# Performance work log

Measured on AMD Instinct MI355X. Metric: run time of the kernel, lower is better.

## Reference

```python
import jax, jax.numpy as jnp
import numpy as np

VOCAB_SIZES = [100000] * 26
EMBED_DIM = 128
BOT_DIMS = [512, 256, 128]
TOP_DIMS = [1024, 1024, 512, 256, 1]
N_DENSE = 13
BATCH = 8192


def setup_inputs() -> dict:
    key = jax.random.key(0)
    ks = jax.random.split(key, 32)
    inp = {}
    inp['dense_features'] = jax.random.normal(ks[0], (BATCH, N_DENSE), dtype=jnp.float32)
    inp['cat_features'] = jax.random.randint(ks[1], (BATCH, 26), 0, VOCAB_SIZES[0], dtype=jnp.int32)
    total_vocab = sum(VOCAB_SIZES)
    inp['embedding_table'] = jax.random.uniform(ks[2], (total_vocab, EMBED_DIM), dtype=jnp.float32,
                                               minval=-1.0, maxval=1.0) * (3.0 / EMBED_DIM) ** 0.5
    # Bottom MLP params
    fan_in = N_DENSE
    for i, d in enumerate(BOT_DIMS):
        inp[f'W{i}'] = jax.random.normal(ks[3 + i], (fan_in, d), dtype=jnp.float32) * (2.0 / (fan_in + d)) ** 0.5
        inp[f'b{i}'] = jax.random.normal(ks[8 + i], (d,), dtype=jnp.float32) * (1.0 / d) ** 0.5
        fan_in = d
    # Top MLP params; input dim = 128 + 27*28/2 = 506
    n_feat = 1 + len(VOCAB_SIZES)
    fan_in = BOT_DIMS[-1] + n_feat * (n_feat + 1) // 2
    for i, d in enumerate(TOP_DIMS):
        inp[f'T{i}'] = jax.random.normal(ks[14 + i], (fan_in, d), dtype=jnp.float32) * (2.0 / (fan_in + d)) ** 0.5
        inp[f'tb{i}'] = jax.random.normal(ks[22 + i], (d,), dtype=jnp.float32) * (1.0 / d) ** 0.5
        fan_in = d
    return inp


def reference(dense_features, cat_features, embedding_table,
              W0, b0, W1, b1, W2, b2,
              T0, tb0, T1, tb1, T2, tb2, T3, tb3, T4, tb4):
    B = dense_features.shape[0]
    # Bottom MLP
    x = dense_features
    for W, b in ((W0, b0), (W1, b1), (W2, b2)):
        x = jax.nn.relu(x @ W + b)
    bot_out = x  # [B, 128]
    feature_stack = bot_out.reshape(B, -1, EMBED_DIM)  # [B, 1, 128]
    # Embedding lookup with per-table offsets into concatenated table
    offsets = jnp.asarray(np.concatenate([[0], np.cumsum(VOCAB_SIZES[:-1])]), dtype=jnp.int32)
    idx = (cat_features + offsets[None, :]).reshape(-1)
    embed = embedding_table[idx].reshape(B, len(VOCAB_SIZES), EMBED_DIM)  # [B, 26, 128]
    feats = jnp.concatenate([feature_stack, embed], axis=1)  # [B, 27, 128]
    # Dot interaction: upper-triangular (incl. diag) entries of feats @ feats^T
    xactions = jnp.einsum('bnd,bmd->bnm', feats, feats)  # [B, 27, 27]
    iu, ju = jnp.triu_indices(feats.shape[1])
    dot_out = xactions[:, iu, ju]  # [B, 378] row-major upper-tri, same order as boolean-mask extraction
    top_in = jnp.concatenate([bot_out, dot_out], axis=-1)  # [B, 506]
    # Top MLP: relu on all but last layer, sigmoid on last
    tops = ((T0, tb0), (T1, tb1), (T2, tb2), (T3, tb3), (T4, tb4))
    x = top_in
    for i, (W, b) in enumerate(tops):
        x = x @ W + b
        x = jax.nn.sigmoid(x) if i == len(tops) - 1 else jax.nn.relu(x)
    return x
```

## Files before the change

kernel.cpp:

```cpp
#include <hip/hip_runtime.h>
#include <hip/hip_bf16.h>
#include <math.h>

#define BATCH 8192

typedef __bf16 bf16x8 __attribute__((ext_vector_type(8)));
typedef float f32x4 __attribute__((ext_vector_type(4)));

__device__ __forceinline__ unsigned short f2bf(float f) {
    unsigned int u = __float_as_uint(f);
    u = u + 0x7FFFu + ((u >> 16) & 1u);
    return (unsigned short)(u >> 16);
}
__device__ __forceinline__ float bf2f(unsigned short h) {
    return __uint_as_float(((unsigned int)h) << 16);
}
__device__ __forceinline__ void async16(const void* g, void* l) {
    __builtin_amdgcn_global_load_lds(
        (const __attribute__((address_space(1))) unsigned int*)g,
        (__attribute__((address_space(3))) unsigned int*)l, 16, 0, 0);
}

__global__ __launch_bounds__(256) void bottom13_kernel(
    const float* __restrict__ dense,
    const float* __restrict__ W0, const float* __restrict__ b0,
    unsigned short* __restrict__ h1)
{
    __shared__ float xs[8][16];
    const int t = threadIdx.x;
    const int row0 = blockIdx.x * 8;

    if (t < 8 * 13) {
        int r = t / 13, k = t % 13;
        xs[r][k] = dense[(size_t)(row0 + r) * 13 + k];
    }
    __syncthreads();

    #pragma unroll
    for (int jj = 0; jj < 2; ++jj) {
        const int j = t + jj * 256;
        float acc[8];
        const float bj = b0[j];
        #pragma unroll
        for (int r = 0; r < 8; ++r) acc[r] = bj;
        #pragma unroll
        for (int k = 0; k < 13; ++k) {
            float w = W0[k * 512 + j];
            #pragma unroll
            for (int r = 0; r < 8; ++r) acc[r] += xs[r][k] * w;
        }
        #pragma unroll
        for (int r = 0; r < 8; ++r)
            h1[(size_t)(row0 + r) * 512 + j] = f2bf(fmaxf(acc[r], 0.f));
    }
}

struct TransDesc { const float* W; unsigned short* Wt; int K, N, nkb, tile0; };
struct TransDescs { TransDesc d[6]; };

__global__ __launch_bounds__(256) void trans_all_kernel(TransDescs td)
{
    __shared__ float tile[32][33];
    const int b = blockIdx.x;
    int i = 0;
    #pragma unroll
    for (int q = 1; q < 6; ++q) if (b >= td.d[q].tile0) i = q;
    const TransDesc D = td.d[i];
    const int tl = b - D.tile0;
    const int kb = (tl % D.nkb) * 32;
    const int nb = (tl / D.nkb) * 32;
    const int Kpad = D.nkb * 32;
    const int tx = threadIdx.x & 31, ty = threadIdx.x >> 5;

    #pragma unroll
    for (int r = 0; r < 32; r += 8) {
        int k = kb + ty + r;
        tile[ty + r][tx] = (k < D.K) ? D.W[(size_t)k * D.N + nb + tx] : 0.f;
    }
    __syncthreads();
    #pragma unroll
    for (int r = 0; r < 32; r += 8) {
        D.Wt[(size_t)(nb + ty + r) * Kpad + kb + tx] = f2bf(tile[tx][ty + r]);
    }
}

__global__ __launch_bounds__(256) void interact_kernel(
    const int* __restrict__ cat,
    const float* __restrict__ table,
    const float* __restrict__ botf,
    unsigned short* __restrict__ A0)
{
    __shared__ float fs[27][132];
    __shared__ int idx[26];

    const int t = threadIdx.x;
    const int row = blockIdx.x;

    if (t < 26) idx[t] = cat[(size_t)row * 26 + t] + t * 100000;
    __syncthreads();

    for (int q = t; q < 27 * 32; q += 256) {
        const int i  = q >> 5;
        const int c4 = q & 31;
        const float* src = (i == 0) ? (botf + (size_t)row * 128)
                                    : (table + (size_t)idx[i - 1] * 128);
        float4 v = reinterpret_cast<const float4*>(src)[c4];
        fs[i][c4 * 4 + 0] = v.x;
        fs[i][c4 * 4 + 1] = v.y;
        fs[i][c4 * 4 + 2] = v.z;
        fs[i][c4 * 4 + 3] = v.w;
    }
    __syncthreads();

    for (int p = t; p < 378; p += 256) {
        int i = 0, rem = p;
        while (rem >= 27 - i) { rem -= 27 - i; ++i; }
        const int j = i + rem;
        float s = 0.f;
        for (int k = 0; k < 128; k += 4) {
            float4 a = *reinterpret_cast<const float4*>(&fs[i][k]);
            float4 b = *reinterpret_cast<const float4*>(&fs[j][k]);
            s += a.x * b.x + a.y * b.y + a.z * b.z + a.w * b.w;
        }
        A0[(size_t)row * 512 + 128 + p] = f2bf(s);
    }
    if (t < 6) A0[(size_t)row * 512 + 506 + t] = 0;
}

__global__ __launch_bounds__(256) void gemm_bf16_kernel(
    const unsigned short* __restrict__ A,
    const unsigned short* __restrict__ Bt,
    const float* __restrict__ bias,
    unsigned short* __restrict__ C,
    float* __restrict__ Cf,
    int K, int N, int ldc, int relu)
{
    __shared__ unsigned short As[2][128 * 64];
    __shared__ unsigned short Bs[2][128 * 64];

    const int t = threadIdx.x;
    const int lane = t & 63;
    const int wid = t >> 6;
    const int wr = wid >> 1, wc = wid & 1;
    const int row0 = blockIdx.x * 128;
    const int col0 = blockIdx.y * 128;

    const char* gA[4]; const char* gB[4];
    int ldst[4];
    #pragma unroll
    for (int q = 0; q < 4; ++q) {
        int l16 = q * 256 + t;
        int row = l16 >> 3, chunk = l16 & 7;
        int swz = chunk ^ (row & 7);
        gA[q] = (const char*)A  + ((size_t)(row0 + row) * K + swz * 8) * 2;
        gB[q] = (const char*)Bt + ((size_t)(col0 + row) * K + swz * 8) * 2;
        ldst[q] = l16 * 16;
    }

    const int kb = lane >> 4;
    const int r15 = lane & 15;
    int aoff[4][2], boff[4][2];
    #pragma unroll
    for (int m = 0; m < 4; ++m) {
        int r = wr * 64 + m * 16 + r15;
        int c = wc * 64 + m * 16 + r15;
        #pragma unroll
        for (int ks = 0; ks < 2; ++ks) {
            aoff[m][ks] = r * 128 + (((ks * 4 + kb) ^ (r & 7)) << 4);
            boff[m][ks] = c * 128 + (((ks * 4 + kb) ^ (c & 7)) << 4);
        }
    }

    f32x4 acc[4][4] = {};

    const int nt = K >> 6;

    #pragma unroll
    for (int q = 0; q < 4; ++q) {
        async16(gA[q], (char*)As[0] + ldst[q]);
        async16(gB[q], (char*)Bs[0] + ldst[q]);
    }
    __syncthreads();

    int cur = 0;
    for (int tt = 0; tt < nt; ++tt) {
        if (tt + 1 < nt) {
            const size_t koff = (size_t)(tt + 1) * 64 * 2;
            #pragma unroll
            for (int q = 0; q < 4; ++q) {
                async16(gA[q] + koff, (char*)As[cur ^ 1] + ldst[q]);
                async16(gB[q] + koff, (char*)Bs[cur ^ 1] + ldst[q]);
            }
        }

        const char* aB = (const char*)As[cur];
        const char* bB = (const char*)Bs[cur];
        #pragma unroll
        for (int ks = 0; ks < 2; ++ks) {
            bf16x8 af[4], bfr[4];
            #pragma unroll
            for (int m = 0; m < 4; ++m)
                af[m] = *reinterpret_cast<const bf16x8*>(aB + aoff[m][ks]);
            #pragma unroll
            for (int n = 0; n < 4; ++n)
                bfr[n] = *reinterpret_cast<const bf16x8*>(bB + boff[n][ks]);

            #pragma unroll
            for (int m = 0; m < 4; ++m)
                #pragma unroll
                for (int n = 0; n < 4; ++n)
                    acc[m][n] = __builtin_amdgcn_mfma_f32_16x16x32_bf16(
                        af[m], bfr[n], acc[m][n], 0, 0, 0);
        }
        __syncthreads();
        cur ^= 1;
    }

    #pragma unroll
    for (int n = 0; n < 4; ++n) {
        const int col_g = col0 + wc * 64 + n * 16 + r15;
        const float bn = bias[col_g];
        #pragma unroll
        for (int m = 0; m < 4; ++m) {
            const int row_base = row0 + wr * 64 + m * 16 + (lane >> 4) * 4;
            #pragma unroll
            for (int reg = 0; reg < 4; ++reg) {
                float v = acc[m][n][reg] + bn;
                if (relu) v = fmaxf(v, 0.f);
                C[(size_t)(row_base + reg) * ldc + col_g] = f2bf(v);
                if (Cf) Cf[(size_t)(row_base + reg) * N + col_g] = v;
            }
        }
    }
}

__global__ __launch_bounds__(256) void final_layer_kernel(
    const unsigned short* __restrict__ A,
    const float* __restrict__ T4,
    const float* __restrict__ tb4,
    float* __restrict__ out)
{
    const int t = threadIdx.x;
    const int lane = t & 63;
    const int wave = t >> 6;
    const int row = blockIdx.x * 4 + wave;

    ushort4 a4 = reinterpret_cast<const ushort4*>(A + (size_t)row * 256)[lane];
    float4 w = reinterpret_cast<const float4*>(T4)[lane];
    float s = bf2f(a4.x) * w.x + bf2f(a4.y) * w.y + bf2f(a4.z) * w.z + bf2f(a4.w) * w.w;
    #pragma unroll
    for (int off = 32; off > 0; off >>= 1) s += __shfl_down(s, off, 64);
    if (lane == 0) out[row] = 1.f / (1.f + expf(-(s + tb4[0])));
}

extern "C" void kernel_launch(void* const* d_in, const int* in_sizes, int n_in,
                              void* d_out, int out_size, void* d_ws, size_t ws_size,
                              hipStream_t stream)
{
    const float* dense = (const float*)d_in[0];
    const int*   cat   = (const int*)d_in[1];
    const float* table = (const float*)d_in[2];
    const float* W0 = (const float*)d_in[3];
    const float* b0 = (const float*)d_in[4];
    const float* W1 = (const float*)d_in[5];
    const float* b1 = (const float*)d_in[6];
    const float* W2 = (const float*)d_in[7];
    const float* b2 = (const float*)d_in[8];
    const float* T0 = (const float*)d_in[9];
    const float* tb0 = (const float*)d_in[10];
    const float* T1 = (const float*)d_in[11];
    const float* tb1 = (const float*)d_in[12];
    const float* T2 = (const float*)d_in[13];
    const float* tb2 = (const float*)d_in[14];
    const float* T3 = (const float*)d_in[15];
    const float* tb3 = (const float*)d_in[16];
    const float* T4 = (const float*)d_in[17];
    const float* tb4 = (const float*)d_in[18];
    float* out = (float*)d_out;

    char* ws = (char*)d_ws;
    unsigned short* A0   = (unsigned short*)(ws);
    unsigned short* act1 = (unsigned short*)(ws + (((size_t)8)  << 20));
    unsigned short* act2 = (unsigned short*)(ws + (((size_t)24) << 20));
    float*          botf = (float*)(ws + (((size_t)40) << 20));
    unsigned short* h1   = (unsigned short*)(ws + (((size_t)44) << 20));
    unsigned short* h2   = (unsigned short*)(ws + (((size_t)52) << 20));
    unsigned short* W1t  = (unsigned short*)(ws + (((size_t)56) << 20));
    unsigned short* W2t  = (unsigned short*)(ws + (((size_t)57) << 20));
    unsigned short* T0t  = (unsigned short*)(ws + (((size_t)58) << 20));
    unsigned short* T1t  = (unsigned short*)(ws + (((size_t)60) << 20));
    unsigned short* T2t  = (unsigned short*)(ws + (((size_t)63) << 20));
    unsigned short* T3t  = (unsigned short*)(ws + (((size_t)66) << 20));

    TransDescs td;
    td.d[0] = { W1, W1t,  512,  256, 16,    0 };
    td.d[1] = { W2, W2t,  256,  128,  8,  128 };
    td.d[2] = { T0, T0t,  506, 1024, 16,  160 };
    td.d[3] = { T1, T1t, 1024, 1024, 32,  672 };
    td.d[4] = { T2, T2t, 1024,  512, 32, 1696 };
    td.d[5] = { T3, T3t,  512,  256, 16, 2208 };
    const int total_tiles = 2336;
    hipLaunchKernelGGL(trans_all_kernel, dim3(total_tiles), dim3(256), 0, stream, td);

    hipLaunchKernelGGL(bottom13_kernel, dim3(BATCH / 8), dim3(256), 0, stream,
                       dense, W0, b0, h1);

    hipLaunchKernelGGL(gemm_bf16_kernel, dim3(BATCH / 128, 256 / 128), dim3(256), 0, stream,
                       h1, W1t, b1, h2, (float*)nullptr, 512, 256, 256, 1);

    hipLaunchKernelGGL(gemm_bf16_kernel, dim3(BATCH / 128, 1), dim3(256), 0, stream,
                       h2, W2t, b2, A0, botf, 256, 128, 512, 1);

    hipLaunchKernelGGL(interact_kernel, dim3(BATCH), dim3(256), 0, stream,
                       cat, table, botf, A0);

    hipLaunchKernelGGL(gemm_bf16_kernel, dim3(BATCH / 128, 1024 / 128), dim3(256), 0, stream,
                       A0, T0t, tb0, act1, (float*)nullptr, 512, 1024, 1024, 1);
    hipLaunchKernelGGL(gemm_bf16_kernel, dim3(BATCH / 128, 1024 / 128), dim3(256), 0, stream,
                       act1, T1t, tb1, act2, (float*)nullptr, 1024, 1024, 1024, 1);
    hipLaunchKernelGGL(gemm_bf16_kernel, dim3(BATCH / 128, 512 / 128), dim3(256), 0, stream,
                       act2, T2t, tb2, act1, (float*)nullptr, 1024, 512, 512, 1);
    hipLaunchKernelGGL(gemm_bf16_kernel, dim3(BATCH / 128, 256 / 128), dim3(256), 0, stream,
                       act1, T3t, tb3, act2, (float*)nullptr, 512, 256, 256, 1);

    hipLaunchKernelGGL(final_layer_kernel, dim3(BATCH / 4), dim3(256), 0, stream,
                       act2, T4, tb4, out);
}
```

Before: 149.2 us.

## Merge prep kernels and rework GEMM double-buffer sync with explicit waitcnt

The weight-transpose and bottom-layer-0 kernels are merged into one launch that splits work by block index, removing a launch and letting both run concurrently. The GEMM main loop is restructured: it waits only on the previous tile's loads using vmcnt(8), with raw s_barrier and sched_barrier fences, raises wave priority around the MFMA section, and peels the last iteration. The goal is to overlap the next tile's global-to-LDS loads with compute and cut barrier overhead. It relies on the vmcnt counting being right for correctness.

```diff
diff --git a/kernel.cpp b/kernel.cpp
--- a/kernel.cpp
+++ b/kernel.cpp
@@ -21,66 +21,68 @@
         (__attribute__((address_space(3))) unsigned int*)l, 16, 0, 0);
 }
 
-__global__ __launch_bounds__(256) void bottom13_kernel(
+struct TransDesc { const float* W; unsigned short* Wt; int K, N, nkb, tile0; };
+struct TransDescs { TransDesc d[6]; };
+#define N_TRANS_TILES 2336
+
+__global__ __launch_bounds__(256) void prep_kernel(
+    TransDescs td,
     const float* __restrict__ dense,
     const float* __restrict__ W0, const float* __restrict__ b0,
     unsigned short* __restrict__ h1)
 {
+    __shared__ float tile[32][33];
     __shared__ float xs[8][16];
     const int t = threadIdx.x;
-    const int row0 = blockIdx.x * 8;
-
-    if (t < 8 * 13) {
-        int r = t / 13, k = t % 13;
-        xs[r][k] = dense[(size_t)(row0 + r) * 13 + k];
-    }
-    __syncthreads();
-
-    #pragma unroll
-    for (int jj = 0; jj < 2; ++jj) {
-        const int j = t + jj * 256;
-        float acc[8];
-        const float bj = b0[j];
-        #pragma unroll
-        for (int r = 0; r < 8; ++r) acc[r] = bj;
-        #pragma unroll
-        for (int k = 0; k < 13; ++k) {
-            float w = W0[k * 512 + j];
-            #pragma unroll
-            for (int r = 0; r < 8; ++r) acc[r] += xs[r][k] * w;
-        }
-        #pragma unroll
-        for (int r = 0; r < 8; ++r)
-            h1[(size_t)(row0 + r) * 512 + j] = f2bf(fmaxf(acc[r], 0.f));
-    }
-}
-
-struct TransDesc { const float* W; unsigned short* Wt; int K, N, nkb, tile0; };
-struct TransDescs { TransDesc d[6]; };
-
-__global__ __launch_bounds__(256) void trans_all_kernel(TransDescs td)
-{
-    __shared__ float tile[32][33];
-    const int b = blockIdx.x;
-    int i = 0;
-    #pragma unroll
-    for (int q = 1; q < 6; ++q) if (b >= td.d[q].tile0) i = q;
-    const TransDesc D = td.d[i];
-    const int tl = b - D.tile0;
-    const int kb = (tl % D.nkb) * 32;
-    const int nb = (tl / D.nkb) * 32;
-    const int Kpad = D.nkb * 32;
-    const int tx = threadIdx.x & 31, ty = threadIdx.x >> 5;
-
-    #pragma unroll
-    for (int r = 0; r < 32; r += 8) {
-        int k = kb + ty + r;
-        tile[ty + r][tx] = (k < D.K) ? D.W[(size_t)k * D.N + nb + tx] : 0.f;
-    }
-    __syncthreads();
-    #pragma unroll
-    for (int r = 0; r < 32; r += 8) {
-        D.Wt[(size_t)(nb + ty + r) * Kpad + kb + tx] = f2bf(tile[tx][ty + r]);
+
+    if (blockIdx.x < N_TRANS_TILES) {
+        const int b = blockIdx.x;
+        int i = 0;
+        #pragma unroll
+        for (int q = 1; q < 6; ++q) if (b >= td.d[q].tile0) i = q;
+        const TransDesc D = td.d[i];
+        const int tl = b - D.tile0;
+        const int kb = (tl % D.nkb) * 32;
+        const int nb = (tl / D.nkb) * 32;
+        const int Kpad = D.nkb * 32;
+        const int tx = t & 31, ty = t >> 5;
+
+        #pragma unroll
+        for (int r = 0; r < 32; r += 8) {
+            int k = kb + ty + r;
+            tile[ty + r][tx] = (k < D.K) ? D.W[(size_t)k * D.N + nb + tx] : 0.f;
+        }
+        __syncthreads();
+        #pragma unroll
+        for (int r = 0; r < 32; r += 8) {
+            D.Wt[(size_t)(nb + ty + r) * Kpad + kb + tx] = f2bf(tile[tx][ty + r]);
+        }
+    } else {
+        const int row0 = (blockIdx.x - N_TRANS_TILES) * 8;
+
+        if (t < 8 * 13) {
+            int r = t / 13, k = t % 13;
+            xs[r][k] = dense[(size_t)(row0 + r) * 13 + k];
+        }
+        __syncthreads();
+
+        #pragma unroll
+        for (int jj = 0; jj < 2; ++jj) {
+            const int j = t + jj * 256;
+            float acc[8];
+            const float bj = b0[j];
+            #pragma unroll
+            for (int r = 0; r < 8; ++r) acc[r] = bj;
+            #pragma unroll
+            for (int k = 0; k < 13; ++k) {
+                float w = W0[k * 512 + j];
+                #pragma unroll
+                for (int r = 0; r < 8; ++r) acc[r] += xs[r][k] * w;
+            }
+            #pragma unroll
+            for (int r = 0; r < 8; ++r)
+                h1[(size_t)(row0 + r) * 512 + j] = f2bf(fmaxf(acc[r], 0.f));
+        }
     }
 }
 
@@ -180,19 +182,52 @@
         async16(gA[q], (char*)As[0] + ldst[q]);
         async16(gB[q], (char*)Bs[0] + ldst[q]);
     }
-    __syncthreads();
 
     int cur = 0;
-    for (int tt = 0; tt < nt; ++tt) {
-        if (tt + 1 < nt) {
-            const size_t koff = (size_t)(tt + 1) * 64 * 2;
-            #pragma unroll
-            for (int q = 0; q < 4; ++q) {
-                async16(gA[q] + koff, (char*)As[cur ^ 1] + ldst[q]);
-                async16(gB[q] + koff, (char*)Bs[cur ^ 1] + ldst[q]);
+    for (int tt = 0; tt < nt - 1; ++tt) {
+        const size_t koff = (size_t)(tt + 1) * 128;
+        #pragma unroll
+        for (int q = 0; q < 4; ++q) {
+            async16(gA[q] + koff, (char*)As[cur ^ 1] + ldst[q]);
+            async16(gB[q] + koff, (char*)Bs[cur ^ 1] + ldst[q]);
+        }
+        asm volatile("s_waitcnt vmcnt(8)" ::: "memory");
+        __builtin_amdgcn_s_barrier();
+        __builtin_amdgcn_sched_barrier(0);
+
+        {
+            const char* aB = (const char*)As[cur];
+            const char* bB = (const char*)Bs[cur];
+            __builtin_amdgcn_s_setprio(1);
+            #pragma unroll
+            for (int ks = 0; ks < 2; ++ks) {
+                bf16x8 af[4], bfr[4];
+                #pragma unroll
+                for (int m = 0; m < 4; ++m)
+                    af[m] = *reinterpret_cast<const bf16x8*>(aB + aoff[m][ks]);
+                #pragma unroll
+                for (int n = 0; n < 4; ++n)
+                    bfr[n] = *reinterpret_cast<const bf16x8*>(bB + boff[n][ks]);
+
+                #pragma unroll
+                for (int m = 0; m < 4; ++m)
+                    #pragma unroll
+                    for (int n = 0; n < 4; ++n)
+                        acc[m][n] = __builtin_amdgcn_mfma_f32_16x16x32_bf16(
+                            af[m], bfr[n], acc[m][n], 0, 0, 0);
             }
-        }
-
+            __builtin_amdgcn_s_setprio(0);
+        }
+        __builtin_amdgcn_sched_barrier(0);
+        __builtin_amdgcn_s_barrier();
+        __builtin_amdgcn_sched_barrier(0);
+        cur ^= 1;
+    }
+
+    asm volatile("s_waitcnt vmcnt(0)" ::: "memory");
+    __builtin_amdgcn_s_barrier();
+    __builtin_amdgcn_sched_barrier(0);
+    {
         const char* aB = (const char*)As[cur];
         const char* bB = (const char*)Bs[cur];
         #pragma unroll
@@ -212,8 +247,6 @@
                     acc[m][n] = __builtin_amdgcn_mfma_f32_16x16x32_bf16(
                         af[m], bfr[n], acc[m][n], 0, 0, 0);
         }
-        __syncthreads();
-        cur ^= 1;
     }
 
     #pragma unroll
@@ -299,11 +332,8 @@
     td.d[3] = { T1, T1t, 1024, 1024, 32,  672 };
     td.d[4] = { T2, T2t, 1024,  512, 32, 1696 };
     td.d[5] = { T3, T3t,  512,  256, 16, 2208 };
-    const int total_tiles = 2336;
-    hipLaunchKernelGGL(trans_all_kernel, dim3(total_tiles), dim3(256), 0, stream, td);
-
-    hipLaunchKernelGGL(bottom13_kernel, dim3(BATCH / 8), dim3(256), 0, stream,
-                       dense, W0, b0, h1);
+    hipLaunchKernelGGL(prep_kernel, dim3(N_TRANS_TILES + BATCH / 8), dim3(256), 0, stream,
+                       td, dense, W0, b0, h1);
 
     hipLaunchKernelGGL(gemm_bf16_kernel, dim3(BATCH / 128, 256 / 128), dim3(256), 0, stream,
                        h1, W1t, b1, h2, (float*)nullptr, 512, 256, 256, 1);
```

Result: slower. 153.2 us (+2.7%).

## Merge prep kernels, template GEMM N-tile, drop fp32 bottom output

Applied to the files above, without the earlier changes.

Combines the weight transpose and the first bottom-MLP layer into one launch and templates the GEMM on tile width so the small-N layers use 64-wide tiles and launch more blocks. It also removes the separate fp32 copy of the bottom-MLP output: the interaction kernel now reads that row back from the bf16 A0 buffer. This saves a launch and some global writes, but the bottom features in the dot products now carry bf16 rounding.

```diff
diff --git a/kernel.cpp b/kernel.cpp
--- a/kernel.cpp
+++ b/kernel.cpp
@@ -21,73 +21,74 @@
         (__attribute__((address_space(3))) unsigned int*)l, 16, 0, 0);
 }
 
-__global__ __launch_bounds__(256) void bottom13_kernel(
+struct TransDesc { const float* W; unsigned short* Wt; int K, N, nkb, tile0; };
+struct TransDescs { TransDesc d[6]; };
+#define N_TRANS_TILES 2336
+
+__global__ __launch_bounds__(256) void prep_kernel(
+    TransDescs td,
     const float* __restrict__ dense,
     const float* __restrict__ W0, const float* __restrict__ b0,
     unsigned short* __restrict__ h1)
 {
+    __shared__ float tile[32][33];
     __shared__ float xs[8][16];
     const int t = threadIdx.x;
-    const int row0 = blockIdx.x * 8;
-
-    if (t < 8 * 13) {
-        int r = t / 13, k = t % 13;
-        xs[r][k] = dense[(size_t)(row0 + r) * 13 + k];
-    }
-    __syncthreads();
-
-    #pragma unroll
-    for (int jj = 0; jj < 2; ++jj) {
-        const int j = t + jj * 256;
-        float acc[8];
-        const float bj = b0[j];
-        #pragma unroll
-        for (int r = 0; r < 8; ++r) acc[r] = bj;
-        #pragma unroll
-        for (int k = 0; k < 13; ++k) {
-            float w = W0[k * 512 + j];
-            #pragma unroll
-            for (int r = 0; r < 8; ++r) acc[r] += xs[r][k] * w;
-        }
-        #pragma unroll
-        for (int r = 0; r < 8; ++r)
-            h1[(size_t)(row0 + r) * 512 + j] = f2bf(fmaxf(acc[r], 0.f));
-    }
-}
-
-struct TransDesc { const float* W; unsigned short* Wt; int K, N, nkb, tile0; };
-struct TransDescs { TransDesc d[6]; };
-
-__global__ __launch_bounds__(256) void trans_all_kernel(TransDescs td)
-{
-    __shared__ float tile[32][33];
-    const int b = blockIdx.x;
-    int i = 0;
-    #pragma unroll
-    for (int q = 1; q < 6; ++q) if (b >= td.d[q].tile0) i = q;
-    const TransDesc D = td.d[i];
-    const int tl = b - D.tile0;
-    const int kb = (tl % D.nkb) * 32;
-    const int nb = (tl / D.nkb) * 32;
-    const int Kpad = D.nkb * 32;
-    const int tx = threadIdx.x & 31, ty = threadIdx.x >> 5;
-
-    #pragma unroll
-    for (int r = 0; r < 32; r += 8) {
-        int k = kb + ty + r;
-        tile[ty + r][tx] = (k < D.K) ? D.W[(size_t)k * D.N + nb + tx] : 0.f;
-    }
-    __syncthreads();
-    #pragma unroll
-    for (int r = 0; r < 32; r += 8) {
-        D.Wt[(size_t)(nb + ty + r) * Kpad + kb + tx] = f2bf(tile[tx][ty + r]);
+
+    if (blockIdx.x < N_TRANS_TILES) {
+        const int b = blockIdx.x;
+        int i = 0;
+        #pragma unroll
+        for (int q = 1; q < 6; ++q) if (b >= td.d[q].tile0) i = q;
+        const TransDesc D = td.d[i];
+        const int tl = b - D.tile0;
+        const int kb = (tl % D.nkb) * 32;
+        const int nb = (tl / D.nkb) * 32;
+        const int Kpad = D.nkb * 32;
+        const int tx = t & 31, ty = t >> 5;
+
+        #pragma unroll
+        for (int r = 0; r < 32; r += 8) {
+            int k = kb + ty + r;
+            tile[ty + r][tx] = (k < D.K) ? D.W[(size_t)k * D.N + nb + tx] : 0.f;
+        }
+        __syncthreads();
+        #pragma unroll
+        for (int r = 0; r < 32; r += 8) {
+            D.Wt[(size_t)(nb + ty + r) * Kpad + kb + tx] = f2bf(tile[tx][ty + r]);
+        }
+    } else {
+        const int row0 = (blockIdx.x - N_TRANS_TILES) * 8;
+
+        if (t < 8 * 13) {
+            int r = t / 13, k = t % 13;
+            xs[r][k] = dense[(size_t)(row0 + r) * 13 + k];
+        }
+        __syncthreads();
+
+        #pragma unroll
+        for (int jj = 0; jj < 2; ++jj) {
+            const int j = t + jj * 256;
+            float acc[8];
+            const float bj = b0[j];
+            #pragma unroll
+            for (int r = 0; r < 8; ++r) acc[r] = bj;
+            #pragma unroll
+            for (int k = 0; k < 13; ++k) {
+                float w = W0[k * 512 + j];
+                #pragma unroll
+                for (int r = 0; r < 8; ++r) acc[r] += xs[r][k] * w;
+            }
+            #pragma unroll
+            for (int r = 0; r < 8; ++r)
+                h1[(size_t)(row0 + r) * 512 + j] = f2bf(fmaxf(acc[r], 0.f));
+        }
     }
 }
 
 __global__ __launch_bounds__(256) void interact_kernel(
     const int* __restrict__ cat,
     const float* __restrict__ table,
-    const float* __restrict__ botf,
     unsigned short* __restrict__ A0)
 {
     __shared__ float fs[27][132];
@@ -99,12 +100,17 @@
     if (t < 26) idx[t] = cat[(size_t)row * 26 + t] + t * 100000;
     __syncthreads();
 
-    for (int q = t; q < 27 * 32; q += 256) {
-        const int i  = q >> 5;
+    if (t < 32) {
+        ushort4 u = reinterpret_cast<const ushort4*>(A0 + (size_t)row * 512)[t];
+        fs[0][t * 4 + 0] = bf2f(u.x);
+        fs[0][t * 4 + 1] = bf2f(u.y);
+        fs[0][t * 4 + 2] = bf2f(u.z);
+        fs[0][t * 4 + 3] = bf2f(u.w);
+    }
+    for (int q = t; q < 26 * 32; q += 256) {
+        const int i  = (q >> 5) + 1;
         const int c4 = q & 31;
-        const float* src = (i == 0) ? (botf + (size_t)row * 128)
-                                    : (table + (size_t)idx[i - 1] * 128);
-        float4 v = reinterpret_cast<const float4*>(src)[c4];
+        float4 v = reinterpret_cast<const float4*>(table + (size_t)idx[i - 1] * 128)[c4];
         fs[i][c4 * 4 + 0] = v.x;
         fs[i][c4 * 4 + 1] = v.y;
         fs[i][c4 * 4 + 2] = v.z;
@@ -127,88 +133,100 @@
     if (t < 6) A0[(size_t)row * 512 + 506 + t] = 0;
 }
 
+template<int BN>
 __global__ __launch_bounds__(256) void gemm_bf16_kernel(
     const unsigned short* __restrict__ A,
     const unsigned short* __restrict__ Bt,
     const float* __restrict__ bias,
     unsigned short* __restrict__ C,
-    float* __restrict__ Cf,
-    int K, int N, int ldc, int relu)
-{
+    int K, int ldc, int relu)
+{
+    constexpr int NF = BN / 32;
     __shared__ unsigned short As[2][128 * 64];
-    __shared__ unsigned short Bs[2][128 * 64];
+    __shared__ unsigned short Bs[2][BN * 64];
 
     const int t = threadIdx.x;
     const int lane = t & 63;
     const int wid = t >> 6;
     const int wr = wid >> 1, wc = wid & 1;
     const int row0 = blockIdx.x * 128;
-    const int col0 = blockIdx.y * 128;
-
-    const char* gA[4]; const char* gB[4];
-    int ldst[4];
+    const int col0 = blockIdx.y * BN;
+
+    const char* gA[4]; int ldstA[4];
     #pragma unroll
     for (int q = 0; q < 4; ++q) {
         int l16 = q * 256 + t;
         int row = l16 >> 3, chunk = l16 & 7;
         int swz = chunk ^ (row & 7);
-        gA[q] = (const char*)A  + ((size_t)(row0 + row) * K + swz * 8) * 2;
+        gA[q] = (const char*)A + ((size_t)(row0 + row) * K + swz * 8) * 2;
+        ldstA[q] = l16 * 16;
+    }
+    const char* gB[NF]; int ldstB[NF];
+    #pragma unroll
+    for (int q = 0; q < NF; ++q) {
+        int l16 = q * 256 + t;
+        int row = l16 >> 3, chunk = l16 & 7;
+        int swz = chunk ^ (row & 7);
         gB[q] = (const char*)Bt + ((size_t)(col0 + row) * K + swz * 8) * 2;
-        ldst[q] = l16 * 16;
+        ldstB[q] = l16 * 16;
     }
 
     const int kb = lane >> 4;
     const int r15 = lane & 15;
-    int aoff[4][2], boff[4][2];
+    int aoff[4][2], boff[NF][2];
     #pragma unroll
     for (int m = 0; m < 4; ++m) {
         int r = wr * 64 + m * 16 + r15;
-        int c = wc * 64 + m * 16 + r15;
-        #pragma unroll
-        for (int ks = 0; ks < 2; ++ks) {
+        #pragma unroll
+        for (int ks = 0; ks < 2; ++ks)
             aoff[m][ks] = r * 128 + (((ks * 4 + kb) ^ (r & 7)) << 4);
-            boff[m][ks] = c * 128 + (((ks * 4 + kb) ^ (c & 7)) << 4);
-        }
-    }
-
-    f32x4 acc[4][4] = {};
+    }
+    #pragma unroll
+    for (int n = 0; n < NF; ++n) {
+        int c = wc * (BN / 2) + n * 16 + r15;
+        #pragma unroll
+        for (int ks = 0; ks < 2; ++ks)
+            boff[n][ks] = c * 128 + (((ks * 4 + kb) ^ (c & 7)) << 4);
+    }
+
+    f32x4 acc[4][NF] = {};
 
     const int nt = K >> 6;
 
     #pragma unroll
-    for (int q = 0; q < 4; ++q) {
-        async16(gA[q], (char*)As[0] + ldst[q]);
-        async16(gB[q], (char*)Bs[0] + ldst[q]);
-    }
+    for (int q = 0; q < 4; ++q)  async16(gA[q], (char*)As[0] + ldstA[q]);
+    #pragma unroll
+    for (int q = 0; q < NF; ++q) async16(gB[q], (char*)Bs[0] + ldstB[q]);
     __syncthreads();
 
     int cur = 0;
     for (int tt = 0; tt < nt; ++tt) {
         if (tt + 1 < nt) {
-            const size_t koff = (size_t)(tt + 1) * 64 * 2;
-            #pragma unroll
-            for (int q = 0; q < 4; ++q) {
-                async16(gA[q] + koff, (char*)As[cur ^ 1] + ldst[q]);
-                async16(gB[q] + koff, (char*)Bs[cur ^ 1] + ldst[q]);
-            }
+            const size_t koff = (size_t)(tt + 1) * 128;
+            #pragma unroll
+            for (int q = 0; q < 4; ++q)
+                async16(gA[q] + koff, (char*)As[cur ^ 1] + ldstA[q]);
+            #pragma unroll
+            for (int q = 0; q < NF; ++q)
+                async16(gB[q] + koff, (char*)Bs[cur ^ 1] + ldstB[q]);
         }
 
         const char* aB = (const char*)As[cur];
         const char* bB = (const char*)Bs[cur];
         #pragma unroll
         for (int ks = 0; ks < 2; ++ks) {
-            bf16x8 af[4], bfr[4];
+            bf16x8 af[4], bfr[NF];
             #pragma unroll
             for (int m = 0; m < 4; ++m)
                 af[m] = *reinterpret_cast<const bf16x8*>(aB + aoff[m][ks]);
             #pragma unroll
-            for (int n = 0; n < 4; ++n)
+            for (int n = 0; n < NF; ++n)
                 bfr[n] = *reinterpret_cast<const bf16x8*>(bB + boff[n][ks]);
 
             #pragma unroll
             for (int m = 0; m < 4; ++m)
                 #pragma unroll
-                for (int n = 0; n < 4; ++n)
+                for (int n = 0; n < NF; ++n)
                     acc[m][n] = __builtin_amdgcn_mfma_f32_16x16x32_bf16(
                         af[m], bfr[n], acc[m][n], 0, 0, 0);
         }
@@ -217,8 +235,8 @@
     }
 
     #pragma unroll
-    for (int n = 0; n < 4; ++n) {
-        const int col_g = col0 + wc * 64 + n * 16 + r15;
+    for (int n = 0; n < NF; ++n) {
+        const int col_g = col0 + wc * (BN / 2) + n * 16 + r15;
         const float bn = bias[col_g];
         #pragma unroll
         for (int m = 0; m < 4; ++m) {
@@ -228,7 +246,6 @@
                 float v = acc[m][n][reg] + bn;
                 if (relu) v = fmaxf(v, 0.f);
                 C[(size_t)(row_base + reg) * ldc + col_g] = f2bf(v);
-                if (Cf) Cf[(size_t)(row_base + reg) * N + col_g] = v;
             }
         }
     }
@@ -282,7 +299,6 @@
     unsigned short* A0   = (unsigned short*)(ws);
     unsigned short* act1 = (unsigned short*)(ws + (((size_t)8)  << 20));
     unsigned short* act2 = (unsigned short*)(ws + (((size_t)24) << 20));
-    float*          botf = (float*)(ws + (((size_t)40) << 20));
     unsigned short* h1   = (unsigned short*)(ws + (((size_t)44) << 20));
     unsigned short* h2   = (unsigned short*)(ws + (((size_t)52) << 20));
     unsigned short* W1t  = (unsigned short*)(ws + (((size_t)56) << 20));
@@ -299,29 +315,26 @@
     td.d[3] = { T1, T1t, 1024, 1024, 32,  672 };
     td.d[4] = { T2, T2t, 1024,  512, 32, 1696 };
     td.d[5] = { T3, T3t,  512,  256, 16, 2208 };
-    const int total_tiles = 2336;
-    hipLaunchKernelGGL(trans_all_kernel, dim3(total_tiles), dim3(256), 0, stream, td);
-
-    hipLaunchKernelGGL(bottom13_kernel, dim3(BATCH / 8), dim3(256), 0, stream,
-                       dense, W0, b0, h1);
-
-    hipLaunchKernelGGL(gemm_bf16_kernel, dim3(BATCH / 128, 256 / 128), dim3(256), 0, stream,
-                       h1, W1t, b1, h2, (float*)nullptr, 512, 256, 256, 1);
-
-    hipLaunchKernelGGL(gemm_bf16_kernel, dim3(BATCH / 128, 1), dim3(256), 0, stream,
-                       h2, W2t, b2, A0, botf, 256, 128, 512, 1);
+    hipLaunchKernelGGL(prep_kernel, dim3(N_TRANS_TILES + BATCH / 8), dim3(256), 0, stream,
+                       td, dense, W0, b0, h1);
+
+    hipLaunchKernelGGL((gemm_bf16_kernel<64>), dim3(BATCH / 128, 256 / 64), dim3(256), 0, stream,
+                       h1, W1t, b1, h2, 512, 256, 1);
+
+    hipLaunchKernelGGL((gemm_bf16_kernel<64>), dim3(BATCH / 128, 128 / 64), dim3(256), 0, stream,
+                       h2, W2t, b2, A0, 256, 512, 1);
 
     hipLaunchKernelGGL(interact_kernel, dim3(BATCH), dim3(256), 0, stream,
-                       cat, table, botf, A0);
-
-    hipLaunchKernelGGL(gemm_bf16_kernel, dim3(BATCH / 128, 1024 / 128), dim3(256), 0, stream,
-                       A0, T0t, tb0, act1, (float*)nullptr, 512, 1024, 1024, 1);
-    hipLaunchKernelGGL(gemm_bf16_kernel, dim3(BATCH / 128, 1024 / 128), dim3(256), 0, stream,
-                       act1, T1t, tb1, act2, (float*)nullptr, 1024, 1024, 1024, 1);
-    hipLaunchKernelGGL(gemm_bf16_kernel, dim3(BATCH / 128, 512 / 128), dim3(256), 0, stream,
-                       act2, T2t, tb2, act1, (float*)nullptr, 1024, 512, 512, 1);
-    hipLaunchKernelGGL(gemm_bf16_kernel, dim3(BATCH / 128, 256 / 128), dim3(256), 0, stream,
-                       act1, T3t, tb3, act2, (float*)nullptr, 512, 256, 256, 1);
+                       cat, table, A0);
+
+    hipLaunchKernelGGL((gemm_bf16_kernel<128>), dim3(BATCH / 128, 1024 / 128), dim3(256), 0, stream,
+                       A0, T0t, tb0, act1, 512, 1024, 1);
+    hipLaunchKernelGGL((gemm_bf16_kernel<128>), dim3(BATCH / 128, 1024 / 128), dim3(256), 0, stream,
+                       act1, T1t, tb1, act2, 1024, 1024, 1);
+    hipLaunchKernelGGL((gemm_bf16_kernel<128>), dim3(BATCH / 128, 512 / 128), dim3(256), 0, stream,
+                       act2, T2t, tb2, act1, 1024, 512, 1);
+    hipLaunchKernelGGL((gemm_bf16_kernel<64>), dim3(BATCH / 128, 256 / 64), dim3(256), 0, stream,
+                       act1, T3t, tb3, act2, 512, 256, 1);
 
     hipLaunchKernelGGL(final_layer_kernel, dim3(BATCH / 4), dim3(256), 0, stream,
                        act2, T4, tb4, out);
```

After: 135.9 us. 8.9% less time.
